# Performance work log

Measured on AMD Instinct MI355X. Metric: run time of the kernel, lower is better.

Reference implementation:

```python
import jax, jax.numpy as jnp
import numpy as np

HEADS, DIM_HEAD, NEIGHBORS = 8, 64, 64
REL_DIST_SCALE, REL_DIST_CUTOFF, THETA, EPS = 100.0, 5000.0, 10000.0, 1e-8


def _rotate_half(x):
    # interleaved pairs: (x0,x1),(x2,x3),... -> (-x1,x0),(-x3,x2),...
    xp = x.reshape(*x.shape[:-1], -1, 2)
    a, b = xp[..., 0], xp[..., 1]
    return jnp.stack((-b, a), axis=-1).reshape(x.shape)


def _apply_rotary(t, freqs):
    return t * jnp.cos(freqs) + _rotate_half(t) * jnp.sin(freqs)


def _gelu(x):
    return jax.nn.gelu(x, approximate=False)  # torch nn.GELU default = exact erf


def setup_inputs() -> dict:
    key = jax.random.key(0)
    ks = jax.random.split(key, 12)
    b, n, d, e = 2, 2048, 256, 16
    h, dh = HEADS, DIM_HEAD
    inner = h * dh
    std = 0.02
    return {
        "feats": jax.random.normal(ks[0], (b, n, d), jnp.float32),
        "coors": jax.random.normal(ks[1], (b, n, 3), jnp.float32),
        "edges": jax.random.normal(ks[2], (b, n, n, e), jnp.float32),
        "W_qkv": jax.random.normal(ks[3], (d, inner * 3), jnp.float32) * std,
        "W_out": jax.random.normal(ks[4], (inner, d), jnp.float32) * std,
        "b_out": jnp.zeros((d,), jnp.float32),
        "W_e1": jax.random.normal(ks[5], (h + e, 2 * (h + e)), jnp.float32) * std,
        "b_e1": jnp.zeros((2 * (h + e),), jnp.float32),
        "W_e2": jax.random.normal(ks[6], (2 * (h + e), h), jnp.float32) * std,
        "b_e2": jnp.zeros((h,), jnp.float32),
        "W_c": jax.random.normal(ks[7], (h, h), jnp.float32) * std,
        "b_c": jnp.zeros((h,), jnp.float32),
        "W_g": jax.random.normal(ks[8], (h, h), jnp.float32) * std,
        "b_g": jnp.zeros((h,), jnp.float32),
        "coors_combine": jax.random.normal(ks[9], (h,), jnp.float32),
        "coors_scale": jnp.ones((1,), jnp.float32),
    }


def reference(feats, coors, edges, W_qkv, W_out, b_out, W_e1, b_e1, W_e2, b_e2,
              W_c, b_c, W_g, b_g, coors_combine, coors_scale):
    b, n, d = feats.shape
    h, dh, nn_k = HEADS, DIM_HEAD, NEIGHBORS

    # pairwise relative coordinates / distances (O(n^2) irregular part)
    rel_coors = coors[:, :, None, :] - coors[:, None, :, :]            # b n n 3
    rel_dist = jnp.linalg.norm(rel_coors, axis=-1)                      # b n n

    # topk nearest neighbors (largest=False -> top_k of negated distances)
    _, nbhd_idx = jax.lax.top_k(-rel_dist, nn_k)                        # b n nn

    qkv = feats @ W_qkv                                                 # b n 3*h*dh
    q, k, v = jnp.split(qkv, 3, axis=-1)
    q = q.reshape(b, n, h, dh).transpose(0, 2, 1, 3)                    # b h n dh
    k = k.reshape(b, n, h, dh).transpose(0, 2, 1, 3)
    v = v.reshape(b, n, h, dh).transpose(0, 2, 1, 3)

    # batched_index_select gathers
    k = jax.vmap(lambda kb, ib: kb[:, ib])(k, nbhd_idx)                 # b h n nn dh
    v = jax.vmap(lambda vb, ib: vb[:, ib])(v, nbhd_idx)                 # b h n nn dh
    rel_dist_nb = jnp.take_along_axis(rel_dist, nbhd_idx, axis=2)       # b n nn
    rel_coors_nb = jnp.take_along_axis(rel_coors, nbhd_idx[..., None], axis=2)  # b n nn 3
    edges_nb = jnp.take_along_axis(edges, nbhd_idx[..., None], axis=2)  # b n nn e

    # rotary on relative distances; q's freqs are zeros -> identity rotation (skipped)
    inv_freq = 1.0 / (THETA ** (jnp.arange(0, dh, 2, dtype=jnp.float32) / dh))
    t = jnp.minimum(rel_dist_nb * REL_DIST_SCALE, REL_DIST_CUTOFF)
    freqs = jnp.repeat(t[..., None] * inv_freq, 2, axis=-1)[:, None]    # b 1 n nn dh
    k = _apply_rotary(k, freqs)
    v = _apply_rotary(v, freqs)

    # edges provided -> no 1/sqrt(dh) scale, then edge MLP
    qk = jnp.einsum('bhid,bhijd->bhij', q, k)                           # b h i j
    qk = jnp.transpose(qk, (0, 2, 3, 1))                                # b i j h
    x = jnp.concatenate([qk, edges_nb], axis=-1)                        # b i j (h+e)
    qk = _gelu(x @ W_e1 + b_e1) @ W_e2 + b_e2                           # b i j h

    # coordinate attention branch (coors_mlp = GELU + Linear when edges exist)
    coor_weights = _gelu(qk) @ W_c + b_c                                # b i j h
    coor_attn = jax.nn.softmax(coor_weights, axis=2)                    # softmax over j
    gate = jnp.tanh(qk @ W_g + b_g)                                     # b i j h

    nrm = jnp.linalg.norm(rel_coors_nb, axis=-1, keepdims=True)
    rel_normed = rel_coors_nb / jnp.maximum(nrm, EPS) * coors_scale     # b i j 3

    rel_out = jnp.einsum('bijh,bijc->bich', coor_attn * gate, rel_normed)
    coors_delta = jnp.einsum('bich,h->bic', rel_out, coors_combine)     # b n 3

    # feature attention branch
    attn = jax.nn.softmax(jnp.transpose(qk, (0, 3, 1, 2)), axis=-1)     # b h i j
    out = jnp.einsum('bhij,bhijd->bhid', attn, v)
    out = out.transpose(0, 2, 1, 3).reshape(b, n, h * dh)
    node_out = out @ W_out + b_out                                      # b n d
    return node_out, coors_delta
```

## Files before the change

kernel.cpp:

```cpp
#include <hip/hip_runtime.h>
#include <hip/hip_fp16.h>
#include <math.h>

#define NPTS 2048
#define NB 64
#define H 8
#define DH 64
#define INNER 512

__device__ __forceinline__ float gelu_exact(float x) {
  return 0.5f * x * (1.0f + erff(x * 0.7071067811865475f));
}

__device__ __forceinline__ unsigned int pack_cs(float c, float s) {
  __half2 h = __floats2half2_rn(c, s);
  return *reinterpret_cast<unsigned int*>(&h);
}
__device__ __forceinline__ float2 unpack_cs(unsigned int u) {
  __half2 h = *reinterpret_cast<__half2*>(&u);
  return __half22float2(h);
}
__device__ __forceinline__ float2 h2_to_f2(unsigned int u) {
  __half2 h = *reinterpret_cast<__half2*>(&u);
  return __half22float2(h);
}

__global__ __launch_bounds__(256) void gemm_tiled(const float* __restrict__ A,
                                                  const float* __restrict__ B,
                                                  const float* __restrict__ bias,
                                                  float* __restrict__ C,
                                                  __half* __restrict__ kvh,
                                                  int M, int N, int K) {
  __shared__ float As[16][68];
  __shared__ float Bs[16][68];
  const int tid = threadIdx.x;
  const int tx = tid & 15;
  const int ty = tid >> 4;
  const int n0 = blockIdx.x << 6;
  const int m0 = blockIdx.y << 6;
  const int la_m = tid >> 2;
  const int la_k = (tid & 3) << 2;
  const int lb_k = tid >> 4;
  const int lb_n = (tid & 15) << 2;
  float acc[4][4] = {{0.f}};
  for (int kk = 0; kk < K; kk += 16) {
    const float4 a4 = *(const float4*)(A + (size_t)(m0 + la_m) * K + kk + la_k);
    const float4 b4 = *(const float4*)(B + (size_t)(kk + lb_k) * N + n0 + lb_n);
    As[la_k + 0][la_m] = a4.x;
    As[la_k + 1][la_m] = a4.y;
    As[la_k + 2][la_m] = a4.z;
    As[la_k + 3][la_m] = a4.w;
    *(float4*)(&Bs[lb_k][lb_n]) = b4;
    __syncthreads();
#pragma unroll
    for (int k = 0; k < 16; ++k) {
      const float4 av = *(const float4*)(&As[k][ty << 2]);
      const float4 bv = *(const float4*)(&Bs[k][tx << 2]);
      acc[0][0] += av.x * bv.x; acc[0][1] += av.x * bv.y; acc[0][2] += av.x * bv.z; acc[0][3] += av.x * bv.w;
      acc[1][0] += av.y * bv.x; acc[1][1] += av.y * bv.y; acc[1][2] += av.y * bv.z; acc[1][3] += av.y * bv.w;
      acc[2][0] += av.z * bv.x; acc[2][1] += av.z * bv.y; acc[2][2] += av.z * bv.z; acc[2][3] += av.z * bv.w;
      acc[3][0] += av.w * bv.x; acc[3][1] += av.w * bv.y; acc[3][2] += av.w * bv.z; acc[3][3] += av.w * bv.w;
    }
    __syncthreads();
  }
  const bool do_kv = (kvh != nullptr) && (n0 >= 512);
#pragma unroll
  for (int r = 0; r < 4; ++r) {
    const int m = m0 + (ty << 2) + r;
    const int nb = n0 + (tx << 2);
    float v[4];
#pragma unroll
    for (int c = 0; c < 4; ++c) {
      v[c] = acc[r][c];
      if (bias) v[c] += bias[nb + c];
      C[(size_t)m * N + nb + c] = v[c];
    }
    if (do_kv) {
      __half2 h01 = __floats2half2_rn(v[0], v[1]);
      __half2 h23 = __floats2half2_rn(v[2], v[3]);
      uint2 pk;
      pk.x = *reinterpret_cast<unsigned int*>(&h01);
      pk.y = *reinterpret_cast<unsigned int*>(&h23);
      *(uint2*)(kvh + (size_t)m * 1024 + (nb - 512)) = pk;
    }
  }
}

__global__ __launch_bounds__(256, 4) void fused_attn(
    const float* __restrict__ qkv, const __half* __restrict__ kvh,
    const float* __restrict__ coors, const float* __restrict__ edges,
    const float* __restrict__ W_e1, const float* __restrict__ b_e1,
    const float* __restrict__ W_e2, const float* __restrict__ b_e2,
    const float* __restrict__ W_c, const float* __restrict__ b_c,
    const float* __restrict__ W_g, const float* __restrict__ b_g,
    const float* __restrict__ coors_combine, const float* __restrict__ coors_scale,
    float* __restrict__ attn_out, float* __restrict__ coors_out) {
  __shared__ float q_s[H][68];
  __shared__ unsigned int cs_s[NB][33];
  __shared__ float qk_s[NB][9];
  __shared__ float qk2_s[NB][9];
  __shared__ float attn_s[NB][9];
  __shared__ float edg_s[NB][17];
  __shared__ float rel_s[NB][4];
  __shared__ float dist_s[NB];
  __shared__ int idx_s[NB];
  __shared__ float We1[24 * 48];
  __shared__ float We2[48 * 9];
  __shared__ float be1[48];
  __shared__ float be2[H], bcs[H], bgs[H], ccs[H];
  __shared__ float Wcs[H * H], Wgs[H * H];
  __shared__ float credx[4][3];
  __shared__ unsigned long long list[4][64];

  const int row = blockIdx.x;
  const int b = row >> 11;
  const int tid = threadIdx.x;
  const int lane = tid & 63;
  const int wv = tid >> 6;
  const size_t qbase = (size_t)row * 1536;

  {
    int t0 = tid;
    q_s[t0 >> 6][t0 & 63] = qkv[qbase + t0];
    int t1 = tid + 256;
    q_s[t1 >> 6][t1 & 63] = qkv[qbase + t1];
  }
  for (int t = tid; t < 24 * 48; t += 256) We1[t] = W_e1[t];
  for (int t = tid; t < 48 * H; t += 256) We2[(t >> 3) * 9 + (t & 7)] = W_e2[t];
  if (tid < 48) be1[tid] = b_e1[tid];
  if (tid < H) { be2[tid] = b_e2[tid]; bcs[tid] = b_c[tid]; bgs[tid] = b_g[tid]; ccs[tid] = coors_combine[tid]; }
  if (tid < H * H) { Wcs[tid] = W_c[tid]; Wgs[tid] = W_g[tid]; }

  const float* cb = coors + (size_t)b * NPTS * 3;
  const float cx = coors[(size_t)row * 3 + 0];
  const float cy = coors[(size_t)row * 3 + 1];
  const float cz = coors[(size_t)row * 3 + 2];
  {
    unsigned long long keys[8];
#pragma unroll
    for (int s = 0; s < 8; ++s) {
      const int j = (wv << 9) + (s << 6) + lane;
      const float dx = cx - cb[j * 3 + 0];
      const float dy = cy - cb[j * 3 + 1];
      const float dz = cz - cb[j * 3 + 2];
      const float d = sqrtf(dx * dx + dy * dy + dz * dz);
      keys[s] = (((unsigned long long)__float_as_uint(d)) << 32) | (unsigned long long)j;
    }
#define CAS(a, b)                                                   \
    {                                                               \
      unsigned long long lo = keys[a] < keys[b] ? keys[a] : keys[b];\
      unsigned long long hi = keys[a] < keys[b] ? keys[b] : keys[a];\
      keys[a] = lo; keys[b] = hi;                                   \
    }
    CAS(0, 1) CAS(2, 3) CAS(4, 5) CAS(6, 7)
    CAS(0, 2) CAS(1, 3) CAS(4, 6) CAS(5, 7)
    CAS(1, 2) CAS(5, 6)
    CAS(0, 4) CAS(1, 5) CAS(2, 6) CAS(3, 7)
    CAS(2, 4) CAS(3, 5)
    CAS(1, 2) CAS(3, 4) CAS(5, 6)
#undef CAS
    for (int r = 0; r < NB; ++r) {
      unsigned long long w = keys[0];
#pragma unroll
      for (int off = 32; off > 0; off >>= 1) {
        unsigned long long o = __shfl_xor(w, off, 64);
        w = o < w ? o : w;
      }
      const bool win = (keys[0] == w);
#pragma unroll
      for (int i = 0; i < 7; ++i) keys[i] = win ? keys[i + 1] : keys[i];
      keys[7] = win ? ~0ull : keys[7];
      if (lane == (r & 63)) list[wv][r] = w;
    }
  }
  __syncthreads();

  {
    const unsigned long long c = list[wv][lane];
    int rank = lane;
#pragma unroll
    for (int o = 1; o < 4; ++o) {
      const unsigned long long* L = list[(wv + o) & 3];
      int base = 0;
#pragma unroll
      for (int sz = 32; sz > 0; sz >>= 1)
        if (L[base + sz - 1] < c) base += sz;
      rank += base;
    }
    if (rank < NB) {
      idx_s[rank] = (int)(c & 0xffffffffull);
      dist_s[rank] = __uint_as_float((unsigned int)(c >> 32));
    }
  }
  __syncthreads();

  {
    const size_t ebase = (size_t)row * NPTS * 16;
#pragma unroll
    for (int s = 0; s < 4; ++s) {
      const int p = tid + (s << 8);
      const int j = p >> 4, e = p & 15;
      edg_s[j][e] = edges[ebase + (size_t)idx_s[j] * 16 + e];
    }
  }
  if (tid < NB) {
    const int jj = idx_s[tid];
    const float csc = coors_scale[0];
    const float dx = cx - cb[jj * 3 + 0];
    const float dy = cy - cb[jj * 3 + 1];
    const float dz = cz - cb[jj * 3 + 2];
    const float inv = csc / fmaxf(dist_s[tid], 1e-8f);
    rel_s[tid][0] = dx * inv;
    rel_s[tid][1] = dy * inv;
    rel_s[tid][2] = dz * inv;
  }
#pragma unroll
  for (int s = 0; s < 8; ++s) {
    const int p = tid + (s << 8);
    const int j = p >> 5, m = p & 31;
    const float t = fminf(dist_s[j] * 100.0f, 5000.0f);
    const float invf = __expf(-(float)m * 0.28782313662425575f);
    float sv, cv;
    __sincosf(t * invf, &sv, &cv);
    cs_s[j][m] = pack_cs(cv, sv);
  }
  __syncthreads();

#pragma unroll
  for (int s = 0; s < 2; ++s) {
    const int p = tid + (s << 8);
    const int j = p >> 3, h = p & 7;
    const uint2* krow = (const uint2*)(kvh + ((size_t)b * NPTS + idx_s[j]) * 1024 + h * DH);
    float acc = 0.f;
#pragma unroll
    for (int m4 = 0; m4 < 16; ++m4) {
      const uint2 ku = krow[m4];
      const float2 k01 = h2_to_f2(ku.x);
      const float2 k23 = h2_to_f2(ku.y);
      const float4 qv = *(const float4*)(&q_s[h][m4 << 2]);
      const int m = m4 << 1;
      const float2 c0 = unpack_cs(cs_s[j][m]);
      const float2 c1 = unpack_cs(cs_s[j][m + 1]);
      acc += qv.x * (k01.x * c0.x - k01.y * c0.y) + qv.y * (k01.y * c0.x + k01.x * c0.y) +
             qv.z * (k23.x * c1.x - k23.y * c1.y) + qv.w * (k23.y * c1.x + k23.x * c1.y);
    }
    qk_s[j][h] = acc;
  }
  __syncthreads();

  {
    const int j = tid >> 2, part = tid & 3;
    float hv[12];
#pragma unroll
    for (int l = 0; l < 12; ++l) {
      const int hh = part * 12 + l;
      float a = be1[hh];
#pragma unroll
      for (int r = 0; r < 8; ++r) a += qk_s[j][r] * We1[r * 48 + hh];
#pragma unroll
      for (int r = 0; r < 16; ++r) a += edg_s[j][r] * We1[(8 + r) * 48 + hh];
      hv[l] = gelu_exact(a);
    }
    float p8[8];
#pragma unroll
    for (int h = 0; h < 8; ++h) {
      float a = 0.f;
#pragma unroll
      for (int l = 0; l < 12; ++l) a += hv[l] * We2[(part * 12 + l) * 9 + h];
      a += __shfl_xor(a, 1, 64);
      a += __shfl_xor(a, 2, 64);
      p8[h] = a + be2[h];
    }
    qk2_s[j][(part << 1) + 0] = p8[(part << 1) + 0];
    qk2_s[j][(part << 1) + 1] = p8[(part << 1) + 1];
  }
  __syncthreads();

  {
    float qv[8], ge[8];
#pragma unroll
    for (int r = 0; r < 8; ++r) { qv[r] = qk2_s[lane][r]; ge[r] = gelu_exact(qv[r]); }
    float wpart = 0.f;
#pragma unroll
    for (int hh = 0; hh < 2; ++hh) {
      const int h = (wv << 1) + hh;
      float y = qv[h];
      float my = y;
#pragma unroll
      for (int off = 32; off > 0; off >>= 1) my = fmaxf(my, __shfl_xor(my, off, 64));
      const float e2 = __expf(y - my);
      float s2 = e2;
#pragma unroll
      for (int off = 32; off > 0; off >>= 1) s2 += __shfl_xor(s2, off, 64);
      attn_s[lane][h] = e2 / s2;
      float cwv = bcs[h], gt = bgs[h];
#pragma unroll
      for (int r = 0; r < 8; ++r) {
        cwv += ge[r] * Wcs[r * 8 + h];
        gt += qv[r] * Wgs[r * 8 + h];
      }
      gt = tanhf(gt);
      float mx = cwv;
#pragma unroll
      for (int off = 32; off > 0; off >>= 1) mx = fmaxf(mx, __shfl_xor(mx, off, 64));
      const float e = __expf(cwv - mx);
      float sm = e;
#pragma unroll
      for (int off = 32; off > 0; off >>= 1) sm += __shfl_xor(sm, off, 64);
      wpart += (e / sm) * gt * ccs[h];
    }
    float px = wpart * rel_s[lane][0];
    float py = wpart * rel_s[lane][1];
    float pz = wpart * rel_s[lane][2];
#pragma unroll
    for (int off = 32; off > 0; off >>= 1) {
      px += __shfl_xor(px, off, 64);
      py += __shfl_xor(py, off, 64);
      pz += __shfl_xor(pz, off, 64);
    }
    if (lane == 0) { credx[wv][0] = px; credx[wv][1] = py; credx[wv][2] = pz; }
  }
  __syncthreads();

  if (tid == 0) {
    coors_out[(size_t)row * 3 + 0] = credx[0][0] + credx[1][0] + credx[2][0] + credx[3][0];
    coors_out[(size_t)row * 3 + 1] = credx[0][1] + credx[1][1] + credx[2][1] + credx[3][1];
    coors_out[(size_t)row * 3 + 2] = credx[0][2] + credx[1][2] + credx[2][2] + credx[3][2];
  }

  {
    const int h = tid >> 5, m = tid & 31;
    const size_t off_v = (size_t)(512 + h * DH + (m << 1));
    float o0 = 0.f, o1 = 0.f;
#pragma unroll 8
    for (int j = 0; j < NB; ++j) {
      const unsigned int vu = *(const unsigned int*)(kvh + ((size_t)b * NPTS + idx_s[j]) * 1024 + off_v);
      const float2 v = h2_to_f2(vu);
      const float2 cs = unpack_cs(cs_s[j][m]);
      const float a = attn_s[j][h];
      o0 += a * (v.x * cs.x - v.y * cs.y);
      o1 += a * (v.y * cs.x + v.x * cs.y);
    }
    *(float2*)(attn_out + (size_t)row * INNER + h * DH + (m << 1)) = make_float2(o0, o1);
  }
}

extern "C" void kernel_launch(void* const* d_in, const int* in_sizes, int n_in,
                              void* d_out, int out_size, void* d_ws, size_t ws_size,
                              hipStream_t stream) {
  const float* feats = (const float*)d_in[0];
  const float* coors = (const float*)d_in[1];
  const float* edges = (const float*)d_in[2];
  const float* W_qkv = (const float*)d_in[3];
  const float* W_out = (const float*)d_in[4];
  const float* b_out = (const float*)d_in[5];
  const float* W_e1 = (const float*)d_in[6];
  const float* b_e1 = (const float*)d_in[7];
  const float* W_e2 = (const float*)d_in[8];
  const float* b_e2 = (const float*)d_in[9];
  const float* W_c = (const float*)d_in[10];
  const float* b_c = (const float*)d_in[11];
  const float* W_g = (const float*)d_in[12];
  const float* b_g = (const float*)d_in[13];
  const float* cc = (const float*)d_in[14];
  const float* cscale = (const float*)d_in[15];

  float* out = (float*)d_out;
  float* qkv = (float*)d_ws;
  float* attn_out = qkv + (size_t)4096 * 1536;
  __half* kvh = (__half*)(attn_out + (size_t)4096 * 512);

  gemm_tiled<<<dim3(24, 64), 256, 0, stream>>>(feats, W_qkv, nullptr, qkv, kvh, 4096, 1536, 256);
  fused_attn<<<4096, 256, 0, stream>>>(qkv, kvh, coors, edges,
                                       W_e1, b_e1, W_e2, b_e2, W_c, b_c, W_g, b_g,
                                       cc, cscale, attn_out, out + (size_t)4096 * 256);
  gemm_tiled<<<dim3(4, 64), 256, 0, stream>>>(attn_out, W_out, b_out, out, nullptr, 4096, 256, 512);
}
```

Measured before the change: 909.1 us.

## Replace wave-sort top-k merge with shared histogram radix select

Neighbor selection no longer runs a per-wave sorting network, 64 rounds of shuffle-min extraction and a cross-wave merge. It builds a shared-memory histogram on the top 12 bits of each distance key and finds the bucket that holds the 64th-nearest point with a prefix scan. Candidates below that bucket boundary are compacted into aliased shared memory, and each candidate's exact rank is computed by a brute-force count. This trades many serialized shuffle rounds for atomics and a small quadratic rank pass. The candidate buffer is capped at 544, so a very dense boundary bucket would truncate candidates and could give wrong neighbors.

```diff
diff --git a/kernel.cpp b/kernel.cpp
--- a/kernel.cpp
+++ b/kernel.cpp
@@ -100,7 +100,7 @@
   __shared__ float qk_s[NB][9];
   __shared__ float qk2_s[NB][9];
   __shared__ float attn_s[NB][9];
-  __shared__ float edg_s[NB][17];
+  __shared__ __align__(16) float edg_s[NB][17];
   __shared__ float rel_s[NB][4];
   __shared__ float dist_s[NB];
   __shared__ int idx_s[NB];
@@ -110,7 +110,8 @@
   __shared__ float be2[H], bcs[H], bgs[H], ccs[H];
   __shared__ float Wcs[H * H], Wgs[H * H];
   __shared__ float credx[4][3];
-  __shared__ unsigned long long list[4][64];
+  __shared__ int selB_s;
+  __shared__ int ccnt_s;
 
   const int row = blockIdx.x;
   const int b = row >> 11;
@@ -119,6 +120,11 @@
   const int wv = tid >> 6;
   const size_t qbase = (size_t)row * 1536;
 
+  unsigned int* hist = &cs_s[0][0];
+  unsigned long long* cand = reinterpret_cast<unsigned long long*>(&edg_s[0][0]);
+
+  for (int t = tid; t < 2048; t += 256) hist[t] = 0u;
+  if (tid == 0) ccnt_s = 0;
   {
     int t0 = tid;
     q_s[t0 >> 6][t0 & 63] = qkv[qbase + t0];
@@ -135,61 +141,75 @@
   const float cx = coors[(size_t)row * 3 + 0];
   const float cy = coors[(size_t)row * 3 + 1];
   const float cz = coors[(size_t)row * 3 + 2];
-  {
-    unsigned long long keys[8];
+
+  unsigned long long keys[8];
+#pragma unroll
+  for (int s = 0; s < 8; ++s) {
+    const int j = (s << 8) + tid;
+    const float dx = cx - cb[j * 3 + 0];
+    const float dy = cy - cb[j * 3 + 1];
+    const float dz = cz - cb[j * 3 + 2];
+    const float d = sqrtf(dx * dx + dy * dy + dz * dz);
+    keys[s] = (((unsigned long long)__float_as_uint(d)) << 32) | (unsigned long long)j;
+  }
+  __syncthreads();
+
+#pragma unroll
+  for (int s = 0; s < 8; ++s)
+    atomicAdd(&hist[(unsigned int)(keys[s] >> 52)], 1u);
+  __syncthreads();
+
+  const int hb = tid << 3;
+  int s_t = 0;
+#pragma unroll
+  for (int k = 0; k < 8; ++k) s_t += (int)hist[hb + k];
+  int sc = s_t;
+#pragma unroll
+  for (int off = 1; off < 64; off <<= 1) {
+    const int o = __shfl_up(sc, off, 64);
+    if (lane >= off) sc += o;
+  }
+  if (lane == 63) idx_s[wv] = sc;
+  __syncthreads();
+  int base = 0;
+#pragma unroll
+  for (int w = 0; w < 3; ++w)
+    if (w < wv) base += idx_s[w];
+  const int S = base + sc;
+  if (S >= 64 && S - s_t < 64) {
+    int cum = S - s_t;
+    int bsel = hb + 7;
+#pragma unroll
+    for (int k = 0; k < 8; ++k) {
+      cum += (int)hist[hb + k];
+      if (cum >= 64) { bsel = hb + k; break; }
+    }
+    selB_s = bsel;
+  }
+  __syncthreads();
+
+  {
+    const unsigned long long limit = ((unsigned long long)(selB_s + 1)) << 52;
 #pragma unroll
     for (int s = 0; s < 8; ++s) {
-      const int j = (wv << 9) + (s << 6) + lane;
-      const float dx = cx - cb[j * 3 + 0];
-      const float dy = cy - cb[j * 3 + 1];
-      const float dz = cz - cb[j * 3 + 2];
-      const float d = sqrtf(dx * dx + dy * dy + dz * dz);
-      keys[s] = (((unsigned long long)__float_as_uint(d)) << 32) | (unsigned long long)j;
-    }
-#define CAS(a, b)                                                   \
-    {                                                               \
-      unsigned long long lo = keys[a] < keys[b] ? keys[a] : keys[b];\
-      unsigned long long hi = keys[a] < keys[b] ? keys[b] : keys[a];\
-      keys[a] = lo; keys[b] = hi;                                   \
-    }
-    CAS(0, 1) CAS(2, 3) CAS(4, 5) CAS(6, 7)
-    CAS(0, 2) CAS(1, 3) CAS(4, 6) CAS(5, 7)
-    CAS(1, 2) CAS(5, 6)
-    CAS(0, 4) CAS(1, 5) CAS(2, 6) CAS(3, 7)
-    CAS(2, 4) CAS(3, 5)
-    CAS(1, 2) CAS(3, 4) CAS(5, 6)
-#undef CAS
-    for (int r = 0; r < NB; ++r) {
-      unsigned long long w = keys[0];
-#pragma unroll
-      for (int off = 32; off > 0; off >>= 1) {
-        unsigned long long o = __shfl_xor(w, off, 64);
-        w = o < w ? o : w;
+      if (keys[s] < limit) {
+        const int p = atomicAdd(&ccnt_s, 1);
+        if (p < 544) cand[p] = keys[s];
       }
-      const bool win = (keys[0] == w);
-#pragma unroll
-      for (int i = 0; i < 7; ++i) keys[i] = win ? keys[i + 1] : keys[i];
-      keys[7] = win ? ~0ull : keys[7];
-      if (lane == (r & 63)) list[wv][r] = w;
-    }
-  }
-  __syncthreads();
-
-  {
-    const unsigned long long c = list[wv][lane];
-    int rank = lane;
-#pragma unroll
-    for (int o = 1; o < 4; ++o) {
-      const unsigned long long* L = list[(wv + o) & 3];
-      int base = 0;
-#pragma unroll
-      for (int sz = 32; sz > 0; sz >>= 1)
-        if (L[base + sz - 1] < c) base += sz;
-      rank += base;
-    }
-    if (rank < NB) {
-      idx_s[rank] = (int)(c & 0xffffffffull);
-      dist_s[rank] = __uint_as_float((unsigned int)(c >> 32));
+    }
+  }
+  __syncthreads();
+
+  {
+    const int c = min(ccnt_s, 544);
+    for (int i = tid; i < c; i += 256) {
+      const unsigned long long ki = cand[i];
+      int r = 0;
+      for (int j2 = 0; j2 < c; ++j2) r += (cand[j2] < ki) ? 1 : 0;
+      if (r < 64) {
+        idx_s[r] = (int)(ki & 0xffffffffull);
+        dist_s[r] = __uint_as_float((unsigned int)(ki >> 32));
+      }
     }
   }
   __syncthreads();
```

Result: faster. 820.5 us (-9.7%).
